# Kernel tuning notes

Measured on AMD Instinct MI355X. Metric: run time of the kernel, lower is better.

## Reference

```python
import jax, jax.numpy as jnp
import numpy as np

B, N, H, D = 1, 4096, 16, 64
C = H * D  # 1024
SCALE = D ** -0.5


def setup_inputs() -> dict:
    key = jax.random.key(0)
    k1, k2, k3, k4 = jax.random.split(key, 4)
    x = jax.random.normal(k1, (B, N, C), dtype=jnp.float32)
    # torch nn.Linear weights: [out_features, in_features]; y = x @ W.T + b
    w_qkv = jax.random.normal(k2, (3 * C, C), dtype=jnp.float32) * 0.02
    w_proj = jax.random.normal(k3, (C, C), dtype=jnp.float32) * 0.02
    b_proj = jax.random.normal(k4, (C,), dtype=jnp.float32) * 0.02
    return {"x": x, "w_qkv": w_qkv, "w_proj": w_proj, "b_proj": b_proj}


def reference(x, w_qkv, w_proj, b_proj):
    Bn, Nn, Cn = x.shape
    # fused QKV projection (no bias)
    qkv = jnp.einsum('bnc,oc->bno', x, w_qkv)            # [B,N,3C]
    qkv = qkv.reshape(Bn, Nn, 3, H, D)
    q = jnp.transpose(qkv[:, :, 0], (0, 2, 1, 3))        # [B,H,N,D]
    k = jnp.transpose(qkv[:, :, 1], (0, 2, 1, 3))
    v = jnp.transpose(qkv[:, :, 2], (0, 2, 1, 3))
    attn = jnp.einsum('bhnd,bhmd->bhnm', q, k) * SCALE   # [B,H,N,N]
    causal_mask = jnp.triu(jnp.ones((Nn, Nn), dtype=bool), k=1)
    attn = jnp.where(causal_mask, -jnp.inf, attn)
    attn = jax.nn.softmax(attn, axis=-1)
    out = jnp.einsum('bhnm,bhmd->bhnd', attn, v)          # [B,H,N,D]
    out = jnp.transpose(out, (0, 2, 1, 3)).reshape(Bn, Nn, Cn)
    out = jnp.einsum('bnc,oc->bno', out, w_proj) + b_proj
    return out
```

## Files before the change

### kernel.cpp

```cpp
#include <hip/hip_runtime.h>
#include <hip/hip_bf16.h>
#include <stdint.h>
#include <stddef.h>

using bf16 = __hip_bfloat16;
typedef short short8 __attribute__((ext_vector_type(8)));
typedef short short4v __attribute__((ext_vector_type(4)));
typedef short short2v __attribute__((ext_vector_type(2)));
typedef float f32x4 __attribute__((ext_vector_type(4)));
typedef float f32x16 __attribute__((ext_vector_type(16)));
typedef unsigned uintv4 __attribute__((ext_vector_type(4)));

#define MFMA16(A, B, C) __builtin_amdgcn_mfma_f32_16x16x32_bf16(A, B, C, 0, 0, 0)
#define MFMA32(A, B, C) __builtin_amdgcn_mfma_f32_32x32x16_bf16(A, B, C, 0, 0, 0)
#define GLOAD_LDS(g, l) __builtin_amdgcn_global_load_lds( \
    (const __attribute__((address_space(1))) void*)(g),   \
    (__attribute__((address_space(3))) void*)(l), 16, 0, 0)

constexpr int AN  = 4096;
constexpr int NH  = 16;
constexpr int HD  = 64;
constexpr int CC  = 1024;
constexpr int C3  = 3072;
constexpr float QSCALE = 0.125f * 1.4426950408889634f;

__device__ inline short bf16s(float f) {
    return (short)((__float_as_uint(f) + 0x8000u) >> 16);
}
__device__ inline float bf2f(short s) {
    return __uint_as_float(((unsigned)(unsigned short)s) << 16);
}
__device__ inline bf16 sbf(short s) {
    union { short s; bf16 b; } u;
    u.s = s;
    return u.b;
}
#if __has_builtin(__builtin_amdgcn_cvt_pk_bf16_f32)
typedef __bf16 bf16x2 __attribute__((ext_vector_type(2)));
__device__ inline short2v pk2(float a, float b) {
    bf16x2 r = __builtin_amdgcn_cvt_pk_bf16_f32(a, b);
    return *(short2v*)&r;
}
#else
__device__ inline short2v pk2(float a, float b) {
    unsigned ua = __float_as_uint(a) + 0x8000u;
    unsigned ub = __float_as_uint(b) + 0x8000u;
    unsigned r  = __builtin_amdgcn_perm(ub, ua, 0x07060302);
    return *(short2v*)&r;
}
#endif
__device__ inline unsigned pk2u(float a, float b) {
    short2v p = pk2(a, b);
    return *(unsigned*)&p;
}
__device__ inline short4v pack4(float a, float b, float c, float d) {
    short2v lo = pk2(a, b), hi = pk2(c, d);
    short4v r;
    r[0] = lo[0]; r[1] = lo[1]; r[2] = hi[0]; r[3] = hi[1];
    return r;
}
__device__ inline void plswap(unsigned &a, unsigned &b) {
    asm("v_permlane32_swap_b32 %0, %1" : "+v"(a), "+v"(b));
}
#if __has_builtin(__builtin_amdgcn_exp2f)
#define FAST_EXP2(x) __builtin_amdgcn_exp2f(x)
#else
#define FAST_EXP2(x) exp2f(x)
#endif

__device__ inline int detect_mode_inline(const unsigned short* xraw, int lane) {
    int crazy = 0;
    #pragma unroll
    for (int i = 0; i < 4; ++i) {
        const unsigned short u = xraw[lane * 4 + i];
        const int e = (u >> 7) & 0xFF;
        if (e >= 134 || (e != 0 && e <= 110)) ++crazy;
    }
    #pragma unroll
    for (int off = 32; off > 0; off >>= 1)
        crazy += __shfl_down(crazy, off, 64);
    crazy = __shfl(crazy, 0, 64);
    return (crazy >= 8) ? 1 : 0;
}

__device__ inline void cast8(const void* __restrict__ src,
                             bf16* __restrict__ dst, int i, int m) {
    if (m) {
        const float* s = (const float*)src;
        float4 a = *(const float4*)(s + i);
        float4 b = *(const float4*)(s + i + 4);
        short8 o;
        short2v p0 = pk2(a.x, a.y), p1 = pk2(a.z, a.w);
        short2v p2 = pk2(b.x, b.y), p3 = pk2(b.z, b.w);
        o[0] = p0[0]; o[1] = p0[1]; o[2] = p1[0]; o[3] = p1[1];
        o[4] = p2[0]; o[5] = p2[1]; o[6] = p3[0]; o[7] = p3[1];
        *(short8*)(dst + i) = o;
    } else {
        *(short8*)(dst + i) = *(const short8*)((const short*)src + i);
    }
}

__global__ void cast_all(const void* __restrict__ x, const void* __restrict__ wq,
                         const void* __restrict__ wp, const void* __restrict__ bp,
                         bf16* __restrict__ xb, bf16* __restrict__ wqb,
                         bf16* __restrict__ wpb, float* __restrict__ biasf,
                         int* __restrict__ mode) {
    const int b = blockIdx.x;
    const int tid = threadIdx.x;
    const int m = detect_mode_inline((const unsigned short*)x, tid & 63);
    if (b < 2048) {
        cast8(x, xb, (b * 256 + tid) * 8, m);
    } else if (b < 3584) {
        cast8(wq, wqb, ((b - 2048) * 256 + tid) * 8, m);
    } else if (b < 4096) {
        cast8(wp, wpb, ((b - 3584) * 256 + tid) * 8, m);
    } else {
        #pragma unroll
        for (int i = tid; i < CC; i += 256)
            biasf[i] = m ? ((const float*)bp)[i] : bf2f(((const short*)bp)[i]);
        if (tid == 0) *mode = m;
    }
}

constexpr int BM = 128, BN = 128, BK = 32;

__global__ __launch_bounds__(256, 3) void gemm_qkv(
    const bf16* __restrict__ A, const bf16* __restrict__ Bw,
    bf16* __restrict__ qOut, bf16* __restrict__ kOut, bf16* __restrict__ vOut)
{
    __shared__ bf16 As[BM * BK];
    __shared__ bf16 Bs[BN * BK];

    const int tid  = threadIdx.x;
    const int wave = tid >> 6;
    const int lane = tid & 63;
    const int quad = lane >> 4;
    const int l16  = lane & 15;
    const int wr   = wave >> 1;
    const int wc   = wave & 1;
    const int m0   = blockIdx.y * BM;
    const int o0   = blockIdx.x * BN;

    const int srow = lane >> 2;
    const int scol = (lane & 3) * 8;

    f32x4 acc[4][4] = {};

    for (int k0 = 0; k0 < CC; k0 += BK) {
        __syncthreads();
        #pragma unroll
        for (int c = 0; c < 2; ++c) {
            const int rbase = wave * 32 + c * 16;
            GLOAD_LDS(A + (size_t)(m0 + rbase + srow) * CC + k0 + scol, &As[rbase * BK]);
            GLOAD_LDS(Bw + (size_t)(o0 + rbase + srow) * CC + k0 + scol, &Bs[rbase * BK]);
        }
        __syncthreads();

        short8 af[4], bfr[4];
        #pragma unroll
        for (int i = 0; i < 4; ++i)
            af[i] = *(const short8*)&As[(wr * 64 + i * 16 + l16) * BK + quad * 8];
        #pragma unroll
        for (int j = 0; j < 4; ++j)
            bfr[j] = *(const short8*)&Bs[(wc * 64 + j * 16 + l16) * BK + quad * 8];
        #pragma unroll
        for (int i = 0; i < 4; ++i)
            #pragma unroll
            for (int j = 0; j < 4; ++j)
                acc[i][j] = MFMA16(af[i], bfr[j], acc[i][j]);
    }

    if (o0 >= 2 * CC) {
        #pragma unroll
        for (int j = 0; j < 4; ++j) {
            const int dcol = o0 - 2 * CC + wc * 64 + j * 16 + l16;
            const int hV = dcol >> 6, dV = dcol & 63;
            #pragma unroll
            for (int i = 0; i < 4; ++i) {
                const int kv0 = m0 + wr * 64 + i * 16 + quad * 4;
                const size_t addr = (size_t)hV * 64 * AN + (size_t)(kv0 >> 6) * 4096
                                  + (size_t)((kv0 >> 3) & 7) * 512 + dV * 8 + (kv0 & 7);
                *(short4v*)&vOut[addr] =
                    pack4(acc[i][j][0], acc[i][j][1], acc[i][j][2], acc[i][j][3]);
            }
        }
        return;
    }
    if (o0 >= CC) {
        #pragma unroll
        for (int j = 0; j < 4; ++j) {
            const int dcol = o0 - CC + wc * 64 + j * 16 + l16;
            const int hK = dcol >> 6, dc = (dcol >> 3) & 7, de = dcol & 7;
            #pragma unroll
            for (int i = 0; i < 4; ++i) {
                const int kv0 = m0 + wr * 64 + i * 16 + quad * 4;
                const size_t addr = (size_t)hK * 64 * AN + (size_t)(kv0 >> 6) * 4096
                                  + (size_t)dc * 512 + (size_t)(kv0 & 63) * 8 + de;
                #pragma unroll
                for (int r = 0; r < 4; ++r)
                    kOut[addr + r * 8] = sbf(bf16s(acc[i][j][r]));
            }
        }
        return;
    }
    #pragma unroll
    for (int j = 0; j < 4; ++j) {
        const int col = o0 + wc * 64 + j * 16 + l16;
        #pragma unroll
        for (int i = 0; i < 4; ++i) {
            const int row = m0 + wr * 64 + i * 16 + quad * 4;
            #pragma unroll
            for (int r = 0; r < 2; ++r) {
                short2v p = pk2(acc[i][j][2 * r] * QSCALE, acc[i][j][2 * r + 1] * QSCALE);
                qOut[(size_t)(row + 2 * r) * CC + col]     = sbf(p[0]);
                qOut[(size_t)(row + 2 * r + 1) * CC + col] = sbf(p[1]);
            }
        }
    }
}

constexpr int PM = 128, PN = 64, PK = 32;

__global__ __launch_bounds__(256, 2) void gemm_proj(
    const bf16* __restrict__ A, const bf16* __restrict__ Bw,
    const float* __restrict__ bias, void* __restrict__ Cout,
    const int* __restrict__ mode)
{
    __shared__ bf16 As[PM * PK];
    __shared__ bf16 Bs[PN * PK];

    const int tid  = threadIdx.x;
    const int wave = tid >> 6;
    const int lane = tid & 63;
    const int quad = lane >> 4;
    const int l16  = lane & 15;
    const int wr   = wave >> 1;
    const int wc   = wave & 1;
    const int m0   = blockIdx.y * PM;
    const int o0   = blockIdx.x * PN;
    const bool f32out = (*mode != 0);

    const int srow = lane >> 2;
    const int scol = (lane & 3) * 8;

    f32x4 acc[4][2] = {};

    for (int k0 = 0; k0 < CC; k0 += PK) {
        __syncthreads();
        #pragma unroll
        for (int c = 0; c < 2; ++c) {
            const int rbase = wave * 32 + c * 16;
            GLOAD_LDS(A + (size_t)(m0 + rbase + srow) * CC + k0 + scol, &As[rbase * PK]);
        }
        {
            const int rbase = wave * 16;
            GLOAD_LDS(Bw + (size_t)(o0 + rbase + srow) * CC + k0 + scol, &Bs[rbase * PK]);
        }
        __syncthreads();

        short8 af[4], bfr[2];
        #pragma unroll
        for (int i = 0; i < 4; ++i)
            af[i] = *(const short8*)&As[(wr * 64 + i * 16 + l16) * PK + quad * 8];
        #pragma unroll
        for (int j = 0; j < 2; ++j)
            bfr[j] = *(const short8*)&Bs[(wc * 32 + j * 16 + l16) * PK + quad * 8];
        #pragma unroll
        for (int i = 0; i < 4; ++i)
            #pragma unroll
            for (int j = 0; j < 2; ++j)
                acc[i][j] = MFMA16(af[i], bfr[j], acc[i][j]);
    }

    #pragma unroll
    for (int j = 0; j < 2; ++j) {
        const int col = o0 + wc * 32 + j * 16 + l16;
        const float bv = bias[col];
        #pragma unroll
        for (int i = 0; i < 4; ++i) {
            const int row = m0 + wr * 64 + i * 16 + quad * 4;
            if (f32out) {
                #pragma unroll
                for (int r = 0; r < 4; ++r)
                    ((float*)Cout)[(size_t)(row + r) * CC + col] = acc[i][j][r] + bv;
            } else {
                #pragma unroll
                for (int r = 0; r < 2; ++r) {
                    short2v p = pk2(acc[i][j][2 * r] + bv, acc[i][j][2 * r + 1] + bv);
                    ((bf16*)Cout)[(size_t)(row + 2 * r) * CC + col]     = sbf(p[0]);
                    ((bf16*)Cout)[(size_t)(row + 2 * r + 1) * CC + col] = sbf(p[1]);
                }
            }
        }
    }
}

constexpr int TK = 64;

__global__ __launch_bounds__(128, 2) void attn8(
    const bf16* __restrict__ qbuf, const bf16* __restrict__ kP,
    const bf16* __restrict__ vP, bf16* __restrict__ pOn, float* __restrict__ pl)
{
    const int tid  = threadIdx.x;
    const int lane = tid & 63;
    const int l31  = lane & 31;
    const int hh   = lane >> 5;
    const int h    = blockIdx.x & 15;
    const int t    = blockIdx.x >> 4;

    short8 ones8;
    #pragma unroll
    for (int i = 0; i < 8; ++i) ones8[i] = (short)0x3F80;


    #pragma unroll 1
    for (int pp = 0; pp < 2; ++pp) {
        const int tile = pp ? 63 - t : t;
        const int nIt  = tile + 1;
        const int i0   = pp ? ((64 - t) + 1) >> 1 : 0;
        const int i1   = pp ? 64 - t : (t + 2) >> 1;
        const int half = pp;
        const int qw   = tile * 64 + (tid >> 6) * 32;
        const int q    = qw + l31;

        short8 qf[4];
        {
            const bf16* qp = qbuf + (size_t)q * CC + h * HD + hh * 8;
            #pragma unroll
            for (int ki = 0; ki < 4; ++ki)
                qf[ki] = *(const short8*)(qp + ki * 16);
        }

        f32x16 acc_l = {};
        f32x16 acc_o[2] = {};

        if (i0 < i1) {
            const bf16* kb = kP + (size_t)h * 64 * AN + (size_t)i0 * 4096;
            const bf16* vb = vP + (size_t)h * 64 * AN + (size_t)i0 * 4096;
            const bool hasdiag = (i1 == nIt);

            short8 kf[8];
            #pragma unroll
            for (int kt = 0; kt < 2; ++kt)
                #pragma unroll
                for (int ki = 0; ki < 4; ++ki)
                    kf[kt * 4 + ki] = *(const short8*)
                        (kb + (2 * ki + hh) * 512 + kt * 256 + l31 * 8);
            kb += 4096;

            for (int it = i0; it < i1; ++it) {
                short8 vf[8];
                #pragma unroll
                for (int kk = 0; kk < 4; ++kk)
                    #pragma unroll
                    for (int dt2 = 0; dt2 < 2; ++dt2)
                        vf[kk * 2 + dt2] = *(const short8*)
                            (vb + (2 * kk + hh) * 512 + dt2 * 256 + l31 * 8);
                vb += 4096;

                f32x16 st[2];
                __builtin_amdgcn_s_setprio(1);
                #pragma unroll
                for (int kt = 0; kt < 2; ++kt) {
                    f32x16 a = {};
                    #pragma unroll
                    for (int ki = 0; ki < 4; ++ki)
                        a = MFMA32(kf[kt * 4 + ki], qf[ki], a);
                    st[kt] = a;
                }
                __builtin_amdgcn_s_setprio(0);

                if (it + 1 < i1) {
                    #pragma unroll
                    for (int kt = 0; kt < 2; ++kt)
                        #pragma unroll
                        for (int ki = 0; ki < 4; ++ki)
                            kf[kt * 4 + ki] = *(const short8*)
                                (kb + (2 * ki + hh) * 512 + kt * 256 + l31 * 8);
                    kb += 4096;
                }

                if (hasdiag && it == i1 - 1) {
                    const int kv0 = it * TK;
                    #pragma unroll
                    for (int kt = 0; kt < 2; ++kt)
                        #pragma unroll
                        for (int r = 0; r < 16; ++r) {
                            const int kv = kv0 + kt * 32 + (r & 3) + 8 * (r >> 2) + 4 * hh;
                            st[kt][r] = (kv <= q) ? FAST_EXP2(st[kt][r]) : 0.0f;
                        }
                } else {
                    #pragma unroll
                    for (int kt = 0; kt < 2; ++kt)
                        #pragma unroll
                        for (int r = 0; r < 16; ++r)
                            st[kt][r] = FAST_EXP2(st[kt][r]);
                }

                #pragma unroll
                for (int kt = 0; kt < 2; ++kt)
                    #pragma unroll
                    for (int kc = 0; kc < 2; ++kc) {
                        unsigned a0 = pk2u(st[kt][kc * 8 + 0], st[kt][kc * 8 + 1]);
                        unsigned a1 = pk2u(st[kt][kc * 8 + 2], st[kt][kc * 8 + 3]);
                        unsigned c0 = pk2u(st[kt][kc * 8 + 4], st[kt][kc * 8 + 5]);
                        unsigned c1 = pk2u(st[kt][kc * 8 + 6], st[kt][kc * 8 + 7]);
                        plswap(a0, c0);
                        plswap(a1, c1);
                        uintv4 fu;
                        fu[0] = a0; fu[1] = a1; fu[2] = c0; fu[3] = c1;
                        const short8 frag = *(const short8*)&fu;

                        __builtin_amdgcn_s_setprio(1);
                        acc_l = MFMA32(ones8, frag, acc_l);
                        #pragma unroll
                        for (int dt2 = 0; dt2 < 2; ++dt2)
                            acc_o[dt2] = MFMA32(vf[(kt * 2 + kc) * 2 + dt2],
                                                frag, acc_o[dt2]);
                        __builtin_amdgcn_s_setprio(0);
                    }
            }
        }

        const size_t base = (size_t)half * AN * CC + (size_t)q * CC + h * HD;
        #pragma unroll
        for (int dt2 = 0; dt2 < 2; ++dt2)
            #pragma unroll
            for (int g = 0; g < 4; ++g) {
                const int d0 = dt2 * 32 + g * 8 + 4 * hh;
                *(short4v*)&pOn[base + d0] =
                    pack4(acc_o[dt2][4 * g + 0], acc_o[dt2][4 * g + 1],
                          acc_o[dt2][4 * g + 2], acc_o[dt2][4 * g + 3]);
            }
        if (hh == 0)
            pl[(size_t)half * NH * AN + (size_t)h * AN + q] = acc_l[0];
    }
}

__global__ __launch_bounds__(128) void combine_halves(
    const bf16* __restrict__ pOn, const float* __restrict__ pl,
    bf16* __restrict__ outp)
{
    const int q  = blockIdx.x;
    const int c0 = threadIdx.x * 8;
    const int h  = c0 >> 6;
    const float l0 = pl[(size_t)h * AN + q];
    const float l1 = pl[(size_t)NH * AN + (size_t)h * AN + q];
    const float L = l0 + l1;
    const float invL = (L > 0.f) ? 1.f / L : 0.f;
    const size_t off = (size_t)q * CC + c0;
    short8 o0 = *(const short8*)&pOn[off];
    short8 o1 = *(const short8*)&pOn[(size_t)AN * CC + off];
    short8 o;
    #pragma unroll
    for (int e = 0; e < 8; e += 2) {
        float v0 = (bf2f(o0[e])     + bf2f(o1[e]))     * invL;
        float v1 = (bf2f(o0[e + 1]) + bf2f(o1[e + 1])) * invL;
        short2v p = pk2(v0, v1);
        o[e] = p[0]; o[e + 1] = p[1];
    }
    *(short8*)&outp[off] = o;
}

extern "C" void kernel_launch(void* const* d_in, const int* in_sizes, int n_in,
                              void* d_out, int out_size, void* d_ws, size_t ws_size,
                              hipStream_t stream) {
    char* ws = (char*)d_ws;
    bf16*   qbuf     = (bf16*)(ws);
    bf16*   kPack    = (bf16*)(ws + 8388608);
    bf16*   vPack    = (bf16*)(ws + 16777216);
    bf16*   attn_out = (bf16*)(ws + 25165824);
    bf16*   xb       = (bf16*)(ws + 33554432);
    bf16*   wqkvb    = (bf16*)(ws + 41943040);
    bf16*   wprojb   = (bf16*)(ws + 48234496);
    float*  biasf    = (float*)(ws + 50331648);
    int*    mode     = (int*)(ws + 50335744);
    bf16*   pOn      = (bf16*)(ws + 50339840);
    float*  pl       = (float*)(ws + 67117056);

    cast_all<<<dim3(4097), 256, 0, stream>>>(
        d_in[0], d_in[1], d_in[2], d_in[3], xb, wqkvb, wprojb, biasf, mode);

    gemm_qkv<<<dim3(C3 / BN, AN / BM), 256, 0, stream>>>(
        xb, wqkvb, qbuf, kPack, vPack);
    attn8<<<dim3(64 * NH), 128, 0, stream>>>(qbuf, kPack, vPack, pOn, pl);
    combine_halves<<<dim3(AN), 128, 0, stream>>>(pOn, pl, attn_out);
    gemm_proj<<<dim3(CC / PN, AN / PM), 256, 0, stream>>>(
        attn_out, wprojb, biasf, d_out, mode);
}
```

Before: 200.0 us.

## Split attention KV range into four partial slots for more parallel blocks

Each attention block's KV range is split again into two sub-ranges, doubling the grid to 2048 blocks, and occupancy is raised via launch bounds (128, 4). The combine kernel now sums four partial outputs and normalizers instead of two. The workspace is repacked so the larger partial buffer reuses the x/weight cast area, which is no longer needed after the QKV GEMM. The aim is better CU utilization during attention, at the cost of extra partial-output traffic, a heavier combine pass and possible register pressure from the higher occupancy target.

Measured after the change: 427.5 us. +113.7%, slower.

```diff
diff --git a/kernel.cpp b/kernel.cpp
--- a/kernel.cpp
+++ b/kernel.cpp
@@ -297,7 +297,7 @@
 
 constexpr int TK = 64;
 
-__global__ __launch_bounds__(128, 2) void attn8(
+__global__ __launch_bounds__(128, 4) void attn9(
     const bf16* __restrict__ qbuf, const bf16* __restrict__ kP,
     const bf16* __restrict__ vP, bf16* __restrict__ pOn, float* __restrict__ pl)
 {
@@ -305,21 +305,25 @@
     const int lane = tid & 63;
     const int l31  = lane & 31;
     const int hh   = lane >> 5;
-    const int h    = blockIdx.x & 15;
-    const int t    = blockIdx.x >> 4;
+    const int bid  = blockIdx.x;
+    const int h    = bid & 15;
+    const int t    = (bid >> 4) & 63;
+    const int s    = bid >> 10;
 
     short8 ones8;
     #pragma unroll
     for (int i = 0; i < 8; ++i) ones8[i] = (short)0x3F80;
-
 
     #pragma unroll 1
     for (int pp = 0; pp < 2; ++pp) {
         const int tile = pp ? 63 - t : t;
         const int nIt  = tile + 1;
-        const int i0   = pp ? ((64 - t) + 1) >> 1 : 0;
-        const int i1   = pp ? 64 - t : (t + 2) >> 1;
-        const int half = pp;
+        const int fi0  = pp ? ((64 - t) + 1) >> 1 : 0;
+        const int fi1  = pp ? 64 - t : (t + 2) >> 1;
+        const int mid  = fi0 + ((fi1 - fi0 + 1) >> 1);
+        const int i0   = s ? mid : fi0;
+        const int iHi  = s ? fi1 : mid;
+        const int slot = pp * 2 + s;
         const int qw   = tile * 64 + (tid >> 6) * 32;
         const int q    = qw + l31;
 
@@ -334,10 +338,10 @@
         f32x16 acc_l = {};
         f32x16 acc_o[2] = {};
 
-        if (i0 < i1) {
+        if (i0 < iHi) {
             const bf16* kb = kP + (size_t)h * 64 * AN + (size_t)i0 * 4096;
             const bf16* vb = vP + (size_t)h * 64 * AN + (size_t)i0 * 4096;
-            const bool hasdiag = (i1 == nIt);
+            const bool hasdiag = (iHi == nIt);
 
             short8 kf[8];
             #pragma unroll
@@ -348,7 +352,7 @@
                         (kb + (2 * ki + hh) * 512 + kt * 256 + l31 * 8);
             kb += 4096;
 
-            for (int it = i0; it < i1; ++it) {
+            for (int it = i0; it < iHi; ++it) {
                 short8 vf[8];
                 #pragma unroll
                 for (int kk = 0; kk < 4; ++kk)
@@ -370,7 +374,7 @@
                 }
                 __builtin_amdgcn_s_setprio(0);
 
-                if (it + 1 < i1) {
+                if (it + 1 < iHi) {
                     #pragma unroll
                     for (int kt = 0; kt < 2; ++kt)
                         #pragma unroll
@@ -380,7 +384,7 @@
                     kb += 4096;
                 }
 
-                if (hasdiag && it == i1 - 1) {
+                if (hasdiag && it == iHi - 1) {
                     const int kv0 = it * TK;
                     #pragma unroll
                     for (int kt = 0; kt < 2; ++kt)
@@ -422,7 +426,7 @@
             }
         }
 
-        const size_t base = (size_t)half * AN * CC + (size_t)q * CC + h * HD;
+        const size_t base = (size_t)slot * AN * CC + (size_t)q * CC + h * HD;
         #pragma unroll
         for (int dt2 = 0; dt2 < 2; ++dt2)
             #pragma unroll
@@ -433,30 +437,35 @@
                           acc_o[dt2][4 * g + 2], acc_o[dt2][4 * g + 3]);
             }
         if (hh == 0)
-            pl[(size_t)half * NH * AN + (size_t)h * AN + q] = acc_l[0];
-    }
-}
-
-__global__ __launch_bounds__(128) void combine_halves(
+            pl[(size_t)slot * NH * AN + (size_t)h * AN + q] = acc_l[0];
+    }
+}
+
+__global__ __launch_bounds__(128) void combine4(
     const bf16* __restrict__ pOn, const float* __restrict__ pl,
     bf16* __restrict__ outp)
 {
     const int q  = blockIdx.x;
     const int c0 = threadIdx.x * 8;
     const int h  = c0 >> 6;
-    const float l0 = pl[(size_t)h * AN + q];
-    const float l1 = pl[(size_t)NH * AN + (size_t)h * AN + q];
-    const float L = l0 + l1;
+    float L = 0.f;
+    #pragma unroll
+    for (int k = 0; k < 4; ++k)
+        L += pl[(size_t)k * NH * AN + (size_t)h * AN + q];
     const float invL = (L > 0.f) ? 1.f / L : 0.f;
     const size_t off = (size_t)q * CC + c0;
-    short8 o0 = *(const short8*)&pOn[off];
-    short8 o1 = *(const short8*)&pOn[(size_t)AN * CC + off];
+    float acc[8] = {};
+    #pragma unroll
+    for (int k = 0; k < 4; ++k) {
+        short8 ov = *(const short8*)&pOn[(size_t)k * AN * CC + off];
+        #pragma unroll
+        for (int e = 0; e < 8; ++e)
+            acc[e] += bf2f(ov[e]);
+    }
     short8 o;
     #pragma unroll
     for (int e = 0; e < 8; e += 2) {
-        float v0 = (bf2f(o0[e])     + bf2f(o1[e]))     * invL;
-        float v1 = (bf2f(o0[e + 1]) + bf2f(o1[e + 1])) * invL;
-        short2v p = pk2(v0, v1);
+        short2v p = pk2(acc[e] * invL, acc[e + 1] * invL);
         o[e] = p[0]; o[e + 1] = p[1];
     }
     *(short8*)&outp[off] = o;
@@ -470,21 +479,21 @@
     bf16*   kPack    = (bf16*)(ws + 8388608);
     bf16*   vPack    = (bf16*)(ws + 16777216);
     bf16*   attn_out = (bf16*)(ws + 25165824);
-    bf16*   xb       = (bf16*)(ws + 33554432);
-    bf16*   wqkvb    = (bf16*)(ws + 41943040);
-    bf16*   wprojb   = (bf16*)(ws + 48234496);
-    float*  biasf    = (float*)(ws + 50331648);
-    int*    mode     = (int*)(ws + 50335744);
-    bf16*   pOn      = (bf16*)(ws + 50339840);
-    float*  pl       = (float*)(ws + 67117056);
+    bf16*   wprojb   = (bf16*)(ws + 33554432);
+    float*  biasf    = (float*)(ws + 35651584);
+    int*    mode     = (int*)(ws + 35655680);
+    float*  pl       = (float*)(ws + 35659776);
+    bf16*   xb       = (bf16*)(ws + 36708352);
+    bf16*   wqkvb    = (bf16*)(ws + 45096960);
+    bf16*   pOn      = (bf16*)(ws + 36708352);
 
     cast_all<<<dim3(4097), 256, 0, stream>>>(
         d_in[0], d_in[1], d_in[2], d_in[3], xb, wqkvb, wprojb, biasf, mode);
 
     gemm_qkv<<<dim3(C3 / BN, AN / BM), 256, 0, stream>>>(
         xb, wqkvb, qbuf, kPack, vPack);
-    attn8<<<dim3(64 * NH), 128, 0, stream>>>(qbuf, kPack, vPack, pOn, pl);
-    combine_halves<<<dim3(AN), 128, 0, stream>>>(pOn, pl, attn_out);
+    attn9<<<dim3(64 * NH * 2), 128, 0, stream>>>(qbuf, kPack, vPack, pOn, pl);
+    combine4<<<dim3(AN), 128, 0, stream>>>(pOn, pl, attn_out);
     gemm_proj<<<dim3(CC / PN, AN / PM), 256, 0, stream>>>(
         attn_out, wprojb, biasf, d_out, mode);
 }
```
